# Optimization experiments

Hardware: AMD Instinct MI355X
Metric: run time of the kernel (lower is better)

## Reference

```python
import jax, jax.numpy as jnp
import numpy as np

N_NODES = 100000
N_EDGES = 1600000

def _graph_conv(x, src, dst, W_rel, b_rel, W_root):
    # sum-aggregate source features at destination nodes (PyG GraphConv, aggr='add')
    agg = jax.ops.segment_sum(x[src], dst, num_segments=N_NODES)  # [N, Fin]
    return agg @ W_rel.T + b_rel + x @ W_root.T  # [N, Fout]

def setup_inputs() -> dict:
    key = jax.random.key(0)
    ks = jax.random.split(key, 10)
    x = jax.random.normal(ks[0], (N_NODES, 4), dtype=jnp.float32)
    edge_index = jax.random.randint(ks[1], (2, N_EDGES), 0, N_NODES, dtype=jnp.int32)
    def lin(k, fo, fi):
        return jax.random.normal(k, (fo, fi), dtype=jnp.float32) / np.sqrt(fi)
    return {
        "x": x,
        "edge_index": edge_index,
        "W1_rel": lin(ks[2], 128, 4),
        "b1": jax.random.normal(ks[3], (128,), dtype=jnp.float32) * 0.01,
        "W1_root": lin(ks[4], 128, 4),
        "W2_rel": lin(ks[5], 128, 128),
        "b2": jax.random.normal(ks[6], (128,), dtype=jnp.float32) * 0.01,
        "W2_root": lin(ks[7], 128, 128),
        "Wlin": lin(ks[8], 2, 128),
        "blin": jax.random.normal(ks[9], (2,), dtype=jnp.float32) * 0.01,
    }

def reference(x, edge_index, W1_rel, b1, W1_root, W2_rel, b2, W2_root, Wlin, blin):
    src, dst = edge_index[0], edge_index[1]
    h = jax.nn.relu(_graph_conv(x, src, dst, W1_rel, b1, W1_root))   # [N,128]
    h = jax.nn.relu(_graph_conv(h, src, dst, W2_rel, b2, W2_root))   # [N,128]
    # global_mean_pool with batch = zeros -> mean over all nodes, single graph
    g = jnp.mean(h, axis=0, keepdims=True)                           # [1,128]
    return g @ Wlin.T + blin                                         # [1,2]
```

## Files before the change

### kernel.cpp

```cpp
#include <hip/hip_runtime.h>
#include <cstddef>

#define N_NODES 100000
#define N_EDGES 1600000
#define NCHUNK32 3125
#define BUCK_SHIFT 6
#define BUCK_NODES 64
#define NBUCK 1563
#define EB_CAP 1536
#define BF_EDGES 8192
#define BF_BLOCKS ((N_EDGES + BF_EDGES - 1) / BF_EDGES)

typedef __attribute__((ext_vector_type(8))) short short8;
typedef __attribute__((ext_vector_type(4))) float f32x4;
typedef __attribute__((ext_vector_type(2))) float f32x2;

__device__ __forceinline__ unsigned pack_bf16x2(float a, float b) {
  unsigned ua = __float_as_uint(a); ua += 0x7FFFu + ((ua >> 16) & 1u);
  unsigned ub = __float_as_uint(b); ub += 0x7FFFu + ((ub >> 16) & 1u);
  return (ua >> 16) | (ub & 0xFFFF0000u);
}

__global__ __launch_bounds__(512) void k_init(int* __restrict__ bucket_cursor,
                                              float* __restrict__ gsum,
                                              const float* __restrict__ W2_rel,
                                              const float* __restrict__ W2_root,
                                              unsigned* __restrict__ wbuf) {
  int t = threadIdx.x;
  for (int b = t; b < NBUCK; b += 512) bucket_cursor[b] = b * EB_CAP;
  if (t < 128) gsum[t] = 0.0f;
#pragma unroll
  for (int i = 0; i < 8; ++i) {
    int e = t + i * 512;
    int L = e & 63, T = (e >> 6) & 7, K0 = e >> 9;
    int f = T * 16 + (L & 15);
    int k0 = K0 * 32 + ((L >> 4) << 3);
    const float* wsrc = (k0 < 128) ? (W2_rel + f * 128 + k0)
                                   : (W2_root + f * 128 + (k0 - 128));
    float4 w0 = *(const float4*)(wsrc);
    float4 w1 = *(const float4*)(wsrc + 4);
    unsigned* d = wbuf + e * 4;
    d[0] = pack_bf16x2(w0.x, w0.y);
    d[1] = pack_bf16x2(w0.z, w0.w);
    d[2] = pack_bf16x2(w1.x, w1.y);
    d[3] = pack_bf16x2(w1.z, w1.w);
  }
}

__global__ __launch_bounds__(512) void k_bfill(const int* __restrict__ src,
                                               const int* __restrict__ dst,
                                               int* __restrict__ bucket_cursor,
                                               unsigned* __restrict__ ebuf) {
  __shared__ int lh[NBUCK];
  __shared__ int sub_base[NBUCK];
  __shared__ int cur[NBUCK];
  int t = threadIdx.x;
  for (int b = t; b < NBUCK; b += 512) { lh[b] = 0; cur[b] = 0; }
  __syncthreads();
  int e0 = blockIdx.x * BF_EDGES;
  unsigned pk[16];
  int bk[16];
#pragma unroll
  for (int i = 0; i < 16; ++i) {
    int e = e0 + i * 512 + t;
    bk[i] = -1;
    if (e < N_EDGES) {
      int d = dst[e];
      int b = d >> BUCK_SHIFT;
      bk[i] = b;
      pk[i] = ((unsigned)(d & (BUCK_NODES - 1)) << 17) | (unsigned)src[e];
      atomicAdd(&lh[b], 1);
    }
  }
  __syncthreads();
  for (int b = t; b < NBUCK; b += 512)
    sub_base[b] = (lh[b] > 0) ? atomicAdd(&bucket_cursor[b], lh[b]) : 0;
  __syncthreads();
#pragma unroll
  for (int i = 0; i < 16; ++i) {
    if (bk[i] >= 0) {
      int pos = sub_base[bk[i]] + atomicAdd(&cur[bk[i]], 1);
      if (pos < (bk[i] + 1) * EB_CAP) ebuf[pos] = pk[i];
    }
  }
}

__global__ __launch_bounds__(256) void k_fill2(
    const unsigned* __restrict__ ebuf, const int* __restrict__ bucket_cursor,
    const float* __restrict__ x, const float* __restrict__ W1_rel,
    const float* __restrict__ b1, const float* __restrict__ W1_root,
    int* __restrict__ row_start, int* __restrict__ row_end,
    int* __restrict__ csr_src, unsigned short* __restrict__ h1f8) {
  __shared__ int cnt[BUCK_NODES];
  __shared__ int start[BUCK_NODES];
  __shared__ float sagg[BUCK_NODES * 4];
  __shared__ float sx[BUCK_NODES * 4];
  __shared__ float sWa[8 * 128];
  __shared__ float sb1[128];
  int t = threadIdx.x;
  int b = blockIdx.x;
  int base = b * EB_CAP;
  int nb = bucket_cursor[b] - base;
  if (nb > EB_CAP) nb = EB_CAP;
  int n0 = b << BUCK_SHIFT;

  if (t < 128) {
    float4 wr = *(const float4*)(W1_rel + t * 4);
    float4 wo = *(const float4*)(W1_root + t * 4);
    sWa[0 * 128 + t] = wr.x; sWa[1 * 128 + t] = wr.y;
    sWa[2 * 128 + t] = wr.z; sWa[3 * 128 + t] = wr.w;
    sWa[4 * 128 + t] = wo.x; sWa[5 * 128 + t] = wo.y;
    sWa[6 * 128 + t] = wo.z; sWa[7 * 128 + t] = wo.w;
    sb1[t] = b1[t];
  }
  if (t < BUCK_NODES) {
    cnt[t] = 0;
    float4 xv = make_float4(0.f, 0.f, 0.f, 0.f);
    if (n0 + t < N_NODES) xv = *(const float4*)(x + (size_t)(n0 + t) * 4);
    *(float4*)&sx[t * 4] = xv;
  }
  __syncthreads();

  for (int i = t; i < nb; i += 256) atomicAdd(&cnt[ebuf[base + i] >> 17], 1);
  __syncthreads();
  if (t < 64) {
    int v = cnt[t];
    int incl = v;
#pragma unroll
    for (int off = 1; off < 64; off <<= 1) {
      int nvv = __shfl_up(incl, off);
      if (t >= off) incl += nvv;
    }
    int excl = incl - v;
    start[t] = excl;
    cnt[t] = excl;
    if (n0 + t < N_NODES) row_start[n0 + t] = base + excl;
  }
  __syncthreads();
  for (int i = t; i < nb; i += 256) {
    unsigned e = ebuf[base + i];
    int p = atomicAdd(&cnt[e >> 17], 1);
    csr_src[base + p] = (int)(e & 0x1FFFFu);
  }
  __syncthreads();
  {
    int nd = t >> 2, sub = t & 3;
    int rs = base + start[nd];
    int re = base + cnt[nd];
    float4 acc = make_float4(0.f, 0.f, 0.f, 0.f);
    for (int i = rs + sub; i < re; i += 4) {
      int s = csr_src[i];
      float4 v = *(const float4*)(x + (size_t)s * 4);
      acc.x += v.x; acc.y += v.y; acc.z += v.z; acc.w += v.w;
    }
#pragma unroll
    for (int off = 1; off < 4; off <<= 1) {
      acc.x += __shfl_xor(acc.x, off);
      acc.y += __shfl_xor(acc.y, off);
      acc.z += __shfl_xor(acc.z, off);
      acc.w += __shfl_xor(acc.w, off);
    }
    if (sub == 0) *(float4*)&sagg[nd * 4] = acc;
    if (t < 64 && n0 + t < N_NODES) row_end[n0 + t] = base + cnt[t];
  }
  __syncthreads();

  for (int it = t; it < BUCK_NODES * 64; it += 256) {
    int nd = it >> 6;
    if (n0 + nd >= N_NODES) break;
    int fp = it & 63;
    int f = fp * 2;
    float4 a  = *(float4*)&sagg[nd * 4];
    float4 xv = *(float4*)&sx[nd * 4];
    float v0 = sb1[f]
        + a.x  * sWa[0 * 128 + f] + a.y  * sWa[1 * 128 + f]
        + a.z  * sWa[2 * 128 + f] + a.w  * sWa[3 * 128 + f]
        + xv.x * sWa[4 * 128 + f] + xv.y * sWa[5 * 128 + f]
        + xv.z * sWa[6 * 128 + f] + xv.w * sWa[7 * 128 + f];
    int f1 = f + 1;
    float v1 = sb1[f1]
        + a.x  * sWa[0 * 128 + f1] + a.y  * sWa[1 * 128 + f1]
        + a.z  * sWa[2 * 128 + f1] + a.w  * sWa[3 * 128 + f1]
        + xv.x * sWa[4 * 128 + f1] + xv.y * sWa[5 * 128 + f1]
        + xv.z * sWa[6 * 128 + f1] + xv.w * sWa[7 * 128 + f1];
    float r0 = fmaxf(v0, 0.f), r1 = fmaxf(v1, 0.f);
    h1f8[(size_t)(n0 + nd) * 64 + fp] =
        (unsigned short)__builtin_amdgcn_cvt_pk_fp8_f32(r0, r1, 0, false);
  }
}

__global__ __launch_bounds__(256) void k_pull128(
    const unsigned short* __restrict__ h1f8, const int* __restrict__ row_start,
    const int* __restrict__ row_end, const int* __restrict__ csr_src,
    unsigned* __restrict__ agg2b) {
  int w = (blockIdx.x * 256 + threadIdx.x) >> 6;
  if (w >= N_NODES) return;
  int lane = threadIdx.x & 63;
  int rs = row_start[w], re = row_end[w];
  float ax = 0.f, ay = 0.f;
  for (int chunk = rs; chunk < re; chunk += 64) {
    int nv = min(64, re - chunk);
    int sv = (chunk + lane < re) ? csr_src[chunk + lane] : 0;
    int j = 0;
    for (; j + 4 <= nv; j += 4) {
      int s0 = __shfl(sv, j);
      int s1 = __shfl(sv, j + 1);
      int s2 = __shfl(sv, j + 2);
      int s3 = __shfl(sv, j + 3);
      int u0 = h1f8[(size_t)s0 * 64 + lane];
      int u1 = h1f8[(size_t)s1 * 64 + lane];
      int u2 = h1f8[(size_t)s2 * 64 + lane];
      int u3 = h1f8[(size_t)s3 * 64 + lane];
      f32x2 d0 = __builtin_amdgcn_cvt_pk_f32_fp8(u0, false);
      f32x2 d1 = __builtin_amdgcn_cvt_pk_f32_fp8(u1, false);
      f32x2 d2 = __builtin_amdgcn_cvt_pk_f32_fp8(u2, false);
      f32x2 d3 = __builtin_amdgcn_cvt_pk_f32_fp8(u3, false);
      ax += d0.x + d1.x + d2.x + d3.x;
      ay += d0.y + d1.y + d2.y + d3.y;
    }
    for (; j < nv; ++j) {
      int s0 = __shfl(sv, j);
      int u0 = h1f8[(size_t)s0 * 64 + lane];
      f32x2 d0 = __builtin_amdgcn_cvt_pk_f32_fp8(u0, false);
      ax += d0.x; ay += d0.y;
    }
  }
  agg2b[(size_t)w * 64 + lane] = pack_bf16x2(ax, ay);
}

__global__ __launch_bounds__(256) void k_gemm_pool(
    const unsigned* __restrict__ agg2b_u, const unsigned short* __restrict__ h1f8,
    const unsigned* __restrict__ wbuf_u, const float* __restrict__ b2,
    float* __restrict__ gsum) {
  __shared__ float lgs[128];
  int t = threadIdx.x;
  if (t < 128) lgs[t] = 0.0f;
  __syncthreads();

  int lane = t & 63;
  int gw = blockIdx.x * 4 + (t >> 6);
  int lrow = lane & 15;
  int quad = lane >> 4;
  const unsigned short* agg2b = (const unsigned short*)agg2b_u;
  const unsigned char* h8 = (const unsigned char*)h1f8;
  const short8* wb = (const short8*)wbuf_u;

  float bias[8];
#pragma unroll
  for (int tt = 0; tt < 8; ++tt) bias[tt] = b2[tt * 16 + lrow];
  float csum[8] = {0.f, 0.f, 0.f, 0.f, 0.f, 0.f, 0.f, 0.f};

  if (gw < NCHUNK32) {
    int mbase = gw * 32;

    f32x4 acc[2][8];
#pragma unroll
    for (int mt = 0; mt < 2; ++mt)
#pragma unroll
      for (int tt = 0; tt < 8; ++tt) acc[mt][tt] = (f32x4){0.f, 0.f, 0.f, 0.f};

#pragma unroll
    for (int ks = 0; ks < 4; ++ks) {
      const unsigned short* abase = agg2b + ks * 32 + quad * 8;
      short8 afr[2];
#pragma unroll
      for (int mt = 0; mt < 2; ++mt)
        afr[mt] = *(const short8*)(abase + (size_t)(mbase + mt * 16 + lrow) * 128);
      short8 bfr[8];
#pragma unroll
      for (int tt = 0; tt < 8; ++tt) bfr[tt] = wb[(ks * 8 + tt) * 64 + lane];
#pragma unroll
      for (int mt = 0; mt < 2; ++mt)
#pragma unroll
        for (int tt = 0; tt < 8; ++tt)
          acc[mt][tt] = __builtin_amdgcn_mfma_f32_16x16x32_bf16(
              afr[mt], bfr[tt], acc[mt][tt], 0, 0, 0);
    }
#pragma unroll
    for (int ks = 4; ks < 8; ++ks) {
      short8 afr[2];
#pragma unroll
      for (int mt = 0; mt < 2; ++mt) {
        const uint2* ap = (const uint2*)(h8 + (size_t)(mbase + mt * 16 + lrow) * 128
                                         + (ks - 4) * 32 + quad * 8);
        uint2 u = *ap;
        f32x2 a0 = __builtin_amdgcn_cvt_pk_f32_fp8((int)u.x, false);
        f32x2 a1 = __builtin_amdgcn_cvt_pk_f32_fp8((int)u.x, true);
        f32x2 a2 = __builtin_amdgcn_cvt_pk_f32_fp8((int)u.y, false);
        f32x2 a3 = __builtin_amdgcn_cvt_pk_f32_fp8((int)u.y, true);
        unsigned q0 = pack_bf16x2(a0.x, a0.y);
        unsigned q1 = pack_bf16x2(a1.x, a1.y);
        unsigned q2 = pack_bf16x2(a2.x, a2.y);
        unsigned q3 = pack_bf16x2(a3.x, a3.y);
        unsigned q[4] = {q0, q1, q2, q3};
        afr[mt] = *(short8*)q;
      }
      short8 bfr[8];
#pragma unroll
      for (int tt = 0; tt < 8; ++tt) bfr[tt] = wb[(ks * 8 + tt) * 64 + lane];
#pragma unroll
      for (int mt = 0; mt < 2; ++mt)
#pragma unroll
        for (int tt = 0; tt < 8; ++tt)
          acc[mt][tt] = __builtin_amdgcn_mfma_f32_16x16x32_bf16(
              afr[mt], bfr[tt], acc[mt][tt], 0, 0, 0);
    }

#pragma unroll
    for (int mt = 0; mt < 2; ++mt) {
#pragma unroll
      for (int tt = 0; tt < 8; ++tt) {
        f32x4 v = acc[mt][tt];
        float s = fmaxf(v.x + bias[tt], 0.f) + fmaxf(v.y + bias[tt], 0.f)
                + fmaxf(v.z + bias[tt], 0.f) + fmaxf(v.w + bias[tt], 0.f);
        s += __shfl_xor(s, 16);
        s += __shfl_xor(s, 32);
        csum[tt] += s;
      }
    }
  }
  if (lane < 16) {
#pragma unroll
    for (int tt = 0; tt < 8; ++tt) atomicAdd(&lgs[tt * 16 + lane], csum[tt]);
  }
  __syncthreads();
  if (t < 128) atomicAdd(&gsum[t], lgs[t]);
}

__global__ void k_final(const float* __restrict__ gsum, const float* __restrict__ Wlin,
                        const float* __restrict__ blin, float* __restrict__ out) {
  int lane = threadIdx.x;
  float g0 = gsum[lane];
  float g1 = gsum[lane + 64];
  float s0 = g0 * Wlin[lane]       + g1 * Wlin[lane + 64];
  float s1 = g0 * Wlin[128 + lane] + g1 * Wlin[192 + lane];
#pragma unroll
  for (int off = 32; off > 0; off >>= 1) {
    s0 += __shfl_down(s0, off);
    s1 += __shfl_down(s1, off);
  }
  if (lane == 0) {
    const float inv = 1.0f / (float)N_NODES;
    out[0] = s0 * inv + blin[0];
    out[1] = s1 * inv + blin[1];
  }
}

extern "C" void kernel_launch(void* const* d_in, const int* in_sizes, int n_in,
                              void* d_out, int out_size, void* d_ws, size_t ws_size,
                              hipStream_t stream) {
  const float* x       = (const float*)d_in[0];
  const int*   ei      = (const int*)d_in[1];
  const float* W1_rel  = (const float*)d_in[2];
  const float* b1      = (const float*)d_in[3];
  const float* W1_root = (const float*)d_in[4];
  const float* W2_rel  = (const float*)d_in[5];
  const float* b2      = (const float*)d_in[6];
  const float* W2_root = (const float*)d_in[7];
  const float* Wlin    = (const float*)d_in[8];
  const float* blin    = (const float*)d_in[9];
  const int* src = ei;
  const int* dst = ei + N_EDGES;
  float* out = (float*)d_out;

  char* ws = (char*)d_ws;
  int*            row_start     = (int*)(ws);
  int*            row_end       = (int*)(ws + 400000);
  int*            bucket_cursor = (int*)(ws + 800000);
  float*          gsum          = (float*)(ws + 808192);
  unsigned*       wbuf          = (unsigned*)(ws + 808704);
  int*            csr_src       = (int*)(ws + 874240);
  unsigned*       ebuf          = (unsigned*)(ws + 10477312);
  unsigned short* h1f8          = (unsigned short*)(ws + 20080384);
  unsigned*       agg2b         = (unsigned*)(ws + 32880384);

  k_init <<<1, 512, 0, stream>>>(bucket_cursor, gsum, W2_rel, W2_root, wbuf);
  k_bfill<<<BF_BLOCKS, 512, 0, stream>>>(src, dst, bucket_cursor, ebuf);
  k_fill2<<<NBUCK, 256, 0, stream>>>(ebuf, bucket_cursor, x, W1_rel, b1, W1_root,
                                     row_start, row_end, csr_src, h1f8);
  k_pull128<<<(N_NODES * 64 + 255) / 256, 256, 0, stream>>>(h1f8, row_start, row_end,
                                                            csr_src, agg2b);
  k_gemm_pool<<<(NCHUNK32 + 3) / 4, 256, 0, stream>>>(agg2b, h1f8, wbuf, b2, gsum);
  k_final<<<1, 64, 0, stream>>>(gsum, Wlin, blin, out);
}
```

Baseline: 212.6 us.

## Split pull wave into half-waves with 4-byte gathers; fuse final reduction into GEMM

The neighbor-aggregation kernel now has each half-wave handle a different source edge, with every lane loading 4 fp8 features (uint) instead of 2. The two halves are combined with a cross-half shuffle at the end. This halves the gather instructions per edge and doubles the bytes per load. Separately, the final linear layer moves into the GEMM/pool kernel through a last-block-done atomic counter, which removes one kernel launch at the cost of a threadfence and an atomic per block.

```diff
diff --git a/kernel.cpp b/kernel.cpp
--- a/kernel.cpp
+++ b/kernel.cpp
@@ -4,6 +4,7 @@
 #define N_NODES 100000
 #define N_EDGES 1600000
 #define NCHUNK32 3125
+#define GEMM_BLOCKS ((NCHUNK32 + 3) / 4)
 #define BUCK_SHIFT 6
 #define BUCK_NODES 64
 #define NBUCK 1563
@@ -23,12 +24,14 @@
 
 __global__ __launch_bounds__(512) void k_init(int* __restrict__ bucket_cursor,
                                               float* __restrict__ gsum,
+                                              int* __restrict__ done,
                                               const float* __restrict__ W2_rel,
                                               const float* __restrict__ W2_root,
                                               unsigned* __restrict__ wbuf) {
   int t = threadIdx.x;
   for (int b = t; b < NBUCK; b += 512) bucket_cursor[b] = b * EB_CAP;
   if (t < 128) gsum[t] = 0.0f;
+  if (t == 0) *done = 0;
 #pragma unroll
   for (int i = 0; i < 8; ++i) {
     int e = t + i * 512;
@@ -190,49 +193,79 @@
 }
 
 __global__ __launch_bounds__(256) void k_pull128(
-    const unsigned short* __restrict__ h1f8, const int* __restrict__ row_start,
+    const unsigned* __restrict__ h1f8_u, const int* __restrict__ row_start,
     const int* __restrict__ row_end, const int* __restrict__ csr_src,
-    unsigned* __restrict__ agg2b) {
+    uint2* __restrict__ agg2b) {
   int w = (blockIdx.x * 256 + threadIdx.x) >> 6;
   if (w >= N_NODES) return;
   int lane = threadIdx.x & 63;
+  int half = lane >> 5;
+  int hl = lane & 31;
   int rs = row_start[w], re = row_end[w];
-  float ax = 0.f, ay = 0.f;
+  float a0 = 0.f, a1 = 0.f, a2 = 0.f, a3 = 0.f;
   for (int chunk = rs; chunk < re; chunk += 64) {
     int nv = min(64, re - chunk);
     int sv = (chunk + lane < re) ? csr_src[chunk + lane] : 0;
     int j = 0;
-    for (; j + 4 <= nv; j += 4) {
+    for (; j + 8 <= nv; j += 8) {
+      int s0 = __shfl(sv, j + 0 + half);
+      int s1 = __shfl(sv, j + 2 + half);
+      int s2 = __shfl(sv, j + 4 + half);
+      int s3 = __shfl(sv, j + 6 + half);
+      unsigned u0 = h1f8_u[(size_t)s0 * 32 + hl];
+      unsigned u1 = h1f8_u[(size_t)s1 * 32 + hl];
+      unsigned u2 = h1f8_u[(size_t)s2 * 32 + hl];
+      unsigned u3 = h1f8_u[(size_t)s3 * 32 + hl];
+      f32x2 l0 = __builtin_amdgcn_cvt_pk_f32_fp8((int)u0, false);
+      f32x2 h0 = __builtin_amdgcn_cvt_pk_f32_fp8((int)u0, true);
+      f32x2 l1 = __builtin_amdgcn_cvt_pk_f32_fp8((int)u1, false);
+      f32x2 h1 = __builtin_amdgcn_cvt_pk_f32_fp8((int)u1, true);
+      f32x2 l2 = __builtin_amdgcn_cvt_pk_f32_fp8((int)u2, false);
+      f32x2 h2 = __builtin_amdgcn_cvt_pk_f32_fp8((int)u2, true);
+      f32x2 l3 = __builtin_amdgcn_cvt_pk_f32_fp8((int)u3, false);
+      f32x2 h3 = __builtin_amdgcn_cvt_pk_f32_fp8((int)u3, true);
+      a0 += l0.x + l1.x + l2.x + l3.x;
+      a1 += l0.y + l1.y + l2.y + l3.y;
+      a2 += h0.x + h1.x + h2.x + h3.x;
+      a3 += h0.y + h1.y + h2.y + h3.y;
+    }
+    for (; j + 2 <= nv; j += 2) {
+      int s0 = __shfl(sv, j + half);
+      unsigned u0 = h1f8_u[(size_t)s0 * 32 + hl];
+      f32x2 l0 = __builtin_amdgcn_cvt_pk_f32_fp8((int)u0, false);
+      f32x2 h0 = __builtin_amdgcn_cvt_pk_f32_fp8((int)u0, true);
+      a0 += l0.x; a1 += l0.y; a2 += h0.x; a3 += h0.y;
+    }
+    if (j < nv) {
       int s0 = __shfl(sv, j);
-      int s1 = __shfl(sv, j + 1);
-      int s2 = __shfl(sv, j + 2);
-      int s3 = __shfl(sv, j + 3);
-      int u0 = h1f8[(size_t)s0 * 64 + lane];
-      int u1 = h1f8[(size_t)s1 * 64 + lane];
-      int u2 = h1f8[(size_t)s2 * 64 + lane];
-      int u3 = h1f8[(size_t)s3 * 64 + lane];
-      f32x2 d0 = __builtin_amdgcn_cvt_pk_f32_fp8(u0, false);
-      f32x2 d1 = __builtin_amdgcn_cvt_pk_f32_fp8(u1, false);
-      f32x2 d2 = __builtin_amdgcn_cvt_pk_f32_fp8(u2, false);
-      f32x2 d3 = __builtin_amdgcn_cvt_pk_f32_fp8(u3, false);
-      ax += d0.x + d1.x + d2.x + d3.x;
-      ay += d0.y + d1.y + d2.y + d3.y;
-    }
-    for (; j < nv; ++j) {
-      int s0 = __shfl(sv, j);
-      int u0 = h1f8[(size_t)s0 * 64 + lane];
-      f32x2 d0 = __builtin_amdgcn_cvt_pk_f32_fp8(u0, false);
-      ax += d0.x; ay += d0.y;
-    }
-  }
-  agg2b[(size_t)w * 64 + lane] = pack_bf16x2(ax, ay);
+      unsigned u0 = h1f8_u[(size_t)s0 * 32 + hl];
+      if (half == 0) {
+        f32x2 l0 = __builtin_amdgcn_cvt_pk_f32_fp8((int)u0, false);
+        f32x2 h0 = __builtin_amdgcn_cvt_pk_f32_fp8((int)u0, true);
+        a0 += l0.x; a1 += l0.y; a2 += h0.x; a3 += h0.y;
+      }
+    }
+  }
+  a0 += __shfl_xor(a0, 32);
+  a1 += __shfl_xor(a1, 32);
+  a2 += __shfl_xor(a2, 32);
+  a3 += __shfl_xor(a3, 32);
+  if (half == 0) {
+    uint2 o;
+    o.x = pack_bf16x2(a0, a1);
+    o.y = pack_bf16x2(a2, a3);
+    agg2b[(size_t)w * 32 + hl] = o;
+  }
 }
 
 __global__ __launch_bounds__(256) void k_gemm_pool(
     const unsigned* __restrict__ agg2b_u, const unsigned short* __restrict__ h1f8,
     const unsigned* __restrict__ wbuf_u, const float* __restrict__ b2,
-    float* __restrict__ gsum) {
+    float* __restrict__ gsum, int* __restrict__ done,
+    const float* __restrict__ Wlin, const float* __restrict__ blin,
+    float* __restrict__ out) {
   __shared__ float lgs[128];
+  __shared__ int amlast;
   int t = threadIdx.x;
   if (t < 128) lgs[t] = 0.0f;
   __syncthreads();
@@ -288,11 +321,8 @@
         f32x2 a1 = __builtin_amdgcn_cvt_pk_f32_fp8((int)u.x, true);
         f32x2 a2 = __builtin_amdgcn_cvt_pk_f32_fp8((int)u.y, false);
         f32x2 a3 = __builtin_amdgcn_cvt_pk_f32_fp8((int)u.y, true);
-        unsigned q0 = pack_bf16x2(a0.x, a0.y);
-        unsigned q1 = pack_bf16x2(a1.x, a1.y);
-        unsigned q2 = pack_bf16x2(a2.x, a2.y);
-        unsigned q3 = pack_bf16x2(a3.x, a3.y);
-        unsigned q[4] = {q0, q1, q2, q3};
+        unsigned q[4] = {pack_bf16x2(a0.x, a0.y), pack_bf16x2(a1.x, a1.y),
+                         pack_bf16x2(a2.x, a2.y), pack_bf16x2(a3.x, a3.y)};
         afr[mt] = *(short8*)q;
       }
       short8 bfr[8];
@@ -325,24 +355,25 @@
   }
   __syncthreads();
   if (t < 128) atomicAdd(&gsum[t], lgs[t]);
-}
-
-__global__ void k_final(const float* __restrict__ gsum, const float* __restrict__ Wlin,
-                        const float* __restrict__ blin, float* __restrict__ out) {
-  int lane = threadIdx.x;
-  float g0 = gsum[lane];
-  float g1 = gsum[lane + 64];
-  float s0 = g0 * Wlin[lane]       + g1 * Wlin[lane + 64];
-  float s1 = g0 * Wlin[128 + lane] + g1 * Wlin[192 + lane];
-#pragma unroll
-  for (int off = 32; off > 0; off >>= 1) {
-    s0 += __shfl_down(s0, off);
-    s1 += __shfl_down(s1, off);
-  }
-  if (lane == 0) {
-    const float inv = 1.0f / (float)N_NODES;
-    out[0] = s0 * inv + blin[0];
-    out[1] = s1 * inv + blin[1];
+
+  __threadfence();
+  if (t == 0) amlast = (atomicAdd(done, 1) == (int)gridDim.x - 1);
+  __syncthreads();
+  if (amlast && t < 64) {
+    float g0 = atomicAdd(&gsum[t], 0.0f);
+    float g1 = atomicAdd(&gsum[t + 64], 0.0f);
+    float s0 = g0 * Wlin[t]       + g1 * Wlin[t + 64];
+    float s1 = g0 * Wlin[128 + t] + g1 * Wlin[192 + t];
+#pragma unroll
+    for (int off = 32; off > 0; off >>= 1) {
+      s0 += __shfl_down(s0, off);
+      s1 += __shfl_down(s1, off);
+    }
+    if (t == 0) {
+      const float inv = 1.0f / (float)N_NODES;
+      out[0] = s0 * inv + blin[0];
+      out[1] = s1 * inv + blin[1];
+    }
   }
 }
 
@@ -368,18 +399,19 @@
   int*            row_end       = (int*)(ws + 400000);
   int*            bucket_cursor = (int*)(ws + 800000);
   float*          gsum          = (float*)(ws + 808192);
-  unsigned*       wbuf          = (unsigned*)(ws + 808704);
-  int*            csr_src       = (int*)(ws + 874240);
-  unsigned*       ebuf          = (unsigned*)(ws + 10477312);
-  unsigned short* h1f8          = (unsigned short*)(ws + 20080384);
-  unsigned*       agg2b         = (unsigned*)(ws + 32880384);
-
-  k_init <<<1, 512, 0, stream>>>(bucket_cursor, gsum, W2_rel, W2_root, wbuf);
+  int*            done          = (int*)(ws + 808704);
+  unsigned*       wbuf          = (unsigned*)(ws + 808832);
+  int*            csr_src       = (int*)(ws + 874368);
+  unsigned*       ebuf          = (unsigned*)(ws + 10477440);
+  unsigned short* h1f8          = (unsigned short*)(ws + 20080512);
+  uint2*          agg2b         = (uint2*)(ws + 32880512);
+
+  k_init <<<1, 512, 0, stream>>>(bucket_cursor, gsum, done, W2_rel, W2_root, wbuf);
   k_bfill<<<BF_BLOCKS, 512, 0, stream>>>(src, dst, bucket_cursor, ebuf);
   k_fill2<<<NBUCK, 256, 0, stream>>>(ebuf, bucket_cursor, x, W1_rel, b1, W1_root,
                                      row_start, row_end, csr_src, h1f8);
-  k_pull128<<<(N_NODES * 64 + 255) / 256, 256, 0, stream>>>(h1f8, row_start, row_end,
-                                                            csr_src, agg2b);
-  k_gemm_pool<<<(NCHUNK32 + 3) / 4, 256, 0, stream>>>(agg2b, h1f8, wbuf, b2, gsum);
-  k_final<<<1, 64, 0, stream>>>(gsum, Wlin, blin, out);
-}
+  k_pull128<<<(N_NODES * 64 + 255) / 256, 256, 0, stream>>>(
+      (const unsigned*)h1f8, row_start, row_end, csr_src, agg2b);
+  k_gemm_pool<<<GEMM_BLOCKS, 256, 0, stream>>>(
+      (const unsigned*)agg2b, h1f8, wbuf, b2, gsum, done, Wlin, blin, out);
+}
```

Measured after the change: 232.9 us. 1.1x slower.

## Widen gather loads, store aggregated features as fp8, pack row bounds

Applied to the files above, without the earlier changes.

The pull kernel now has each lane load 8 fp8 features (uint2) while four edges are processed per wave at once, then reduces across quarter-waves. The aggregated layer-2 input is stored as fp8 instead of bf16, which halves its write and read traffic in the GEMM, and the GEMM loop is unified over both fp8 operands. Row start/end are packed into an int2, and the edge bucketing kernel reads src/dst with int4 vector loads. The cost is extra precision loss from quantising sums of up to ~16+ fp8 values back to fp8, plus cross-lane shuffles.

```diff
diff --git a/kernel.cpp b/kernel.cpp
--- a/kernel.cpp
+++ b/kernel.cpp
@@ -4,6 +4,7 @@
 #define N_NODES 100000
 #define N_EDGES 1600000
 #define NCHUNK32 3125
+#define GEMM_BLOCKS ((NCHUNK32 + 3) / 4)
 #define BUCK_SHIFT 6
 #define BUCK_NODES 64
 #define NBUCK 1563
@@ -61,15 +62,32 @@
   unsigned pk[16];
   int bk[16];
 #pragma unroll
-  for (int i = 0; i < 16; ++i) {
-    int e = e0 + i * 512 + t;
-    bk[i] = -1;
-    if (e < N_EDGES) {
-      int d = dst[e];
-      int b = d >> BUCK_SHIFT;
-      bk[i] = b;
-      pk[i] = ((unsigned)(d & (BUCK_NODES - 1)) << 17) | (unsigned)src[e];
-      atomicAdd(&lh[b], 1);
+  for (int i = 0; i < 4; ++i) {
+    int e = e0 + (i * 512 + t) * 4;
+    if (e + 4 <= N_EDGES) {
+      int4 s4 = *(const int4*)(src + e);
+      int4 d4 = *(const int4*)(dst + e);
+      int dd[4] = {d4.x, d4.y, d4.z, d4.w};
+      int ss[4] = {s4.x, s4.y, s4.z, s4.w};
+#pragma unroll
+      for (int j = 0; j < 4; ++j) {
+        int b = dd[j] >> BUCK_SHIFT;
+        bk[i * 4 + j] = b;
+        pk[i * 4 + j] = ((unsigned)(dd[j] & (BUCK_NODES - 1)) << 17) | (unsigned)ss[j];
+        atomicAdd(&lh[b], 1);
+      }
+    } else {
+#pragma unroll
+      for (int j = 0; j < 4; ++j) {
+        bk[i * 4 + j] = -1;
+        if (e + j < N_EDGES) {
+          int d = dst[e + j];
+          int b = d >> BUCK_SHIFT;
+          bk[i * 4 + j] = b;
+          pk[i * 4 + j] = ((unsigned)(d & (BUCK_NODES - 1)) << 17) | (unsigned)src[e + j];
+          atomicAdd(&lh[b], 1);
+        }
+      }
     }
   }
   __syncthreads();
@@ -89,8 +107,8 @@
     const unsigned* __restrict__ ebuf, const int* __restrict__ bucket_cursor,
     const float* __restrict__ x, const float* __restrict__ W1_rel,
     const float* __restrict__ b1, const float* __restrict__ W1_root,
-    int* __restrict__ row_start, int* __restrict__ row_end,
-    int* __restrict__ csr_src, unsigned short* __restrict__ h1f8) {
+    int2* __restrict__ row_se, int* __restrict__ csr_src,
+    unsigned short* __restrict__ h1f8) {
   __shared__ int cnt[BUCK_NODES];
   __shared__ int start[BUCK_NODES];
   __shared__ float sagg[BUCK_NODES * 4];
@@ -134,7 +152,6 @@
     int excl = incl - v;
     start[t] = excl;
     cnt[t] = excl;
-    if (n0 + t < N_NODES) row_start[n0 + t] = base + excl;
   }
   __syncthreads();
   for (int i = t; i < nb; i += 256) {
@@ -161,7 +178,8 @@
       acc.w += __shfl_xor(acc.w, off);
     }
     if (sub == 0) *(float4*)&sagg[nd * 4] = acc;
-    if (t < 64 && n0 + t < N_NODES) row_end[n0 + t] = base + cnt[t];
+    if (t < 64 && n0 + t < N_NODES)
+      row_se[n0 + t] = make_int2(base + start[t], base + cnt[t]);
   }
   __syncthreads();
 
@@ -190,46 +208,71 @@
 }
 
 __global__ __launch_bounds__(256) void k_pull128(
-    const unsigned short* __restrict__ h1f8, const int* __restrict__ row_start,
-    const int* __restrict__ row_end, const int* __restrict__ csr_src,
-    unsigned* __restrict__ agg2b) {
+    const unsigned* __restrict__ h1f8_u, const int2* __restrict__ row_se,
+    const int* __restrict__ csr_src, uint2* __restrict__ aggf8) {
   int w = (blockIdx.x * 256 + threadIdx.x) >> 6;
   if (w >= N_NODES) return;
   int lane = threadIdx.x & 63;
-  int rs = row_start[w], re = row_end[w];
-  float ax = 0.f, ay = 0.f;
+  int q = lane >> 4;
+  int ql = lane & 15;
+  int2 se = row_se[w];
+  int rs = se.x, re = se.y;
+  const uint2* hrow = (const uint2*)h1f8_u;
+  float a0=0.f,a1=0.f,a2=0.f,a3=0.f,a4=0.f,a5=0.f,a6=0.f,a7=0.f;
   for (int chunk = rs; chunk < re; chunk += 64) {
     int nv = min(64, re - chunk);
     int sv = (chunk + lane < re) ? csr_src[chunk + lane] : 0;
     int j = 0;
-    for (; j + 4 <= nv; j += 4) {
-      int s0 = __shfl(sv, j);
-      int s1 = __shfl(sv, j + 1);
-      int s2 = __shfl(sv, j + 2);
-      int s3 = __shfl(sv, j + 3);
-      int u0 = h1f8[(size_t)s0 * 64 + lane];
-      int u1 = h1f8[(size_t)s1 * 64 + lane];
-      int u2 = h1f8[(size_t)s2 * 64 + lane];
-      int u3 = h1f8[(size_t)s3 * 64 + lane];
-      f32x2 d0 = __builtin_amdgcn_cvt_pk_f32_fp8(u0, false);
-      f32x2 d1 = __builtin_amdgcn_cvt_pk_f32_fp8(u1, false);
-      f32x2 d2 = __builtin_amdgcn_cvt_pk_f32_fp8(u2, false);
-      f32x2 d3 = __builtin_amdgcn_cvt_pk_f32_fp8(u3, false);
-      ax += d0.x + d1.x + d2.x + d3.x;
-      ay += d0.y + d1.y + d2.y + d3.y;
-    }
-    for (; j < nv; ++j) {
-      int s0 = __shfl(sv, j);
-      int u0 = h1f8[(size_t)s0 * 64 + lane];
-      f32x2 d0 = __builtin_amdgcn_cvt_pk_f32_fp8(u0, false);
-      ax += d0.x; ay += d0.y;
-    }
-  }
-  agg2b[(size_t)w * 64 + lane] = pack_bf16x2(ax, ay);
+    for (; j + 8 <= nv; j += 8) {
+      int sA = __shfl(sv, j + q);
+      int sB = __shfl(sv, j + 4 + q);
+      uint2 uA = hrow[(size_t)sA * 16 + ql];
+      uint2 uB = hrow[(size_t)sB * 16 + ql];
+      f32x2 pA0 = __builtin_amdgcn_cvt_pk_f32_fp8((int)uA.x, false);
+      f32x2 pA1 = __builtin_amdgcn_cvt_pk_f32_fp8((int)uA.x, true);
+      f32x2 pA2 = __builtin_amdgcn_cvt_pk_f32_fp8((int)uA.y, false);
+      f32x2 pA3 = __builtin_amdgcn_cvt_pk_f32_fp8((int)uA.y, true);
+      f32x2 pB0 = __builtin_amdgcn_cvt_pk_f32_fp8((int)uB.x, false);
+      f32x2 pB1 = __builtin_amdgcn_cvt_pk_f32_fp8((int)uB.x, true);
+      f32x2 pB2 = __builtin_amdgcn_cvt_pk_f32_fp8((int)uB.y, false);
+      f32x2 pB3 = __builtin_amdgcn_cvt_pk_f32_fp8((int)uB.y, true);
+      a0 += pA0.x + pB0.x;  a1 += pA0.y + pB0.y;
+      a2 += pA1.x + pB1.x;  a3 += pA1.y + pB1.y;
+      a4 += pA2.x + pB2.x;  a5 += pA2.y + pB2.y;
+      a6 += pA3.x + pB3.x;  a7 += pA3.y + pB3.y;
+    }
+    for (; j < nv; j += 4) {
+      int idx = j + q;
+      int s = __shfl(sv, (idx < nv) ? idx : 0);
+      uint2 u = hrow[(size_t)s * 16 + ql];
+      if (idx >= nv) { u.x = 0u; u.y = 0u; }
+      f32x2 p0 = __builtin_amdgcn_cvt_pk_f32_fp8((int)u.x, false);
+      f32x2 p1 = __builtin_amdgcn_cvt_pk_f32_fp8((int)u.x, true);
+      f32x2 p2 = __builtin_amdgcn_cvt_pk_f32_fp8((int)u.y, false);
+      f32x2 p3 = __builtin_amdgcn_cvt_pk_f32_fp8((int)u.y, true);
+      a0 += p0.x; a1 += p0.y; a2 += p1.x; a3 += p1.y;
+      a4 += p2.x; a5 += p2.y; a6 += p3.x; a7 += p3.y;
+    }
+  }
+  a0 += __shfl_xor(a0, 16); a1 += __shfl_xor(a1, 16);
+  a2 += __shfl_xor(a2, 16); a3 += __shfl_xor(a3, 16);
+  a4 += __shfl_xor(a4, 16); a5 += __shfl_xor(a5, 16);
+  a6 += __shfl_xor(a6, 16); a7 += __shfl_xor(a7, 16);
+  a0 += __shfl_xor(a0, 32); a1 += __shfl_xor(a1, 32);
+  a2 += __shfl_xor(a2, 32); a3 += __shfl_xor(a3, 32);
+  a4 += __shfl_xor(a4, 32); a5 += __shfl_xor(a5, 32);
+  a6 += __shfl_xor(a6, 32); a7 += __shfl_xor(a7, 32);
+  if (lane < 16) {
+    unsigned lo = __builtin_amdgcn_cvt_pk_fp8_f32(a0, a1, 0, false);
+    lo = __builtin_amdgcn_cvt_pk_fp8_f32(a2, a3, lo, true);
+    unsigned hi = __builtin_amdgcn_cvt_pk_fp8_f32(a4, a5, 0, false);
+    hi = __builtin_amdgcn_cvt_pk_fp8_f32(a6, a7, hi, true);
+    aggf8[(size_t)w * 16 + ql] = make_uint2(lo, hi);
+  }
 }
 
 __global__ __launch_bounds__(256) void k_gemm_pool(
-    const unsigned* __restrict__ agg2b_u, const unsigned short* __restrict__ h1f8,
+    const unsigned* __restrict__ aggf8_u, const unsigned short* __restrict__ h1f8,
     const unsigned* __restrict__ wbuf_u, const float* __restrict__ b2,
     float* __restrict__ gsum) {
   __shared__ float lgs[128];
@@ -241,7 +284,7 @@
   int gw = blockIdx.x * 4 + (t >> 6);
   int lrow = lane & 15;
   int quad = lane >> 4;
-  const unsigned short* agg2b = (const unsigned short*)agg2b_u;
+  const unsigned char* g8 = (const unsigned char*)aggf8_u;
   const unsigned char* h8 = (const unsigned char*)h1f8;
   const short8* wb = (const short8*)wbuf_u;
 
@@ -260,40 +303,21 @@
       for (int tt = 0; tt < 8; ++tt) acc[mt][tt] = (f32x4){0.f, 0.f, 0.f, 0.f};
 
 #pragma unroll
-    for (int ks = 0; ks < 4; ++ks) {
-      const unsigned short* abase = agg2b + ks * 32 + quad * 8;
+    for (int ks = 0; ks < 8; ++ks) {
+      const unsigned char* ab = (ks < 4) ? g8 : h8;
+      int koff = (ks & 3) * 32 + quad * 8;
       short8 afr[2];
 #pragma unroll
-      for (int mt = 0; mt < 2; ++mt)
-        afr[mt] = *(const short8*)(abase + (size_t)(mbase + mt * 16 + lrow) * 128);
-      short8 bfr[8];
-#pragma unroll
-      for (int tt = 0; tt < 8; ++tt) bfr[tt] = wb[(ks * 8 + tt) * 64 + lane];
-#pragma unroll
-      for (int mt = 0; mt < 2; ++mt)
-#pragma unroll
-        for (int tt = 0; tt < 8; ++tt)
-          acc[mt][tt] = __builtin_amdgcn_mfma_f32_16x16x32_bf16(
-              afr[mt], bfr[tt], acc[mt][tt], 0, 0, 0);
-    }
-#pragma unroll
-    for (int ks = 4; ks < 8; ++ks) {
-      short8 afr[2];
-#pragma unroll
       for (int mt = 0; mt < 2; ++mt) {
-        const uint2* ap = (const uint2*)(h8 + (size_t)(mbase + mt * 16 + lrow) * 128
-                                         + (ks - 4) * 32 + quad * 8);
+        const uint2* ap = (const uint2*)(ab + (size_t)(mbase + mt * 16 + lrow) * 128 + koff);
         uint2 u = *ap;
         f32x2 a0 = __builtin_amdgcn_cvt_pk_f32_fp8((int)u.x, false);
         f32x2 a1 = __builtin_amdgcn_cvt_pk_f32_fp8((int)u.x, true);
         f32x2 a2 = __builtin_amdgcn_cvt_pk_f32_fp8((int)u.y, false);
         f32x2 a3 = __builtin_amdgcn_cvt_pk_f32_fp8((int)u.y, true);
-        unsigned q0 = pack_bf16x2(a0.x, a0.y);
-        unsigned q1 = pack_bf16x2(a1.x, a1.y);
-        unsigned q2 = pack_bf16x2(a2.x, a2.y);
-        unsigned q3 = pack_bf16x2(a3.x, a3.y);
-        unsigned q[4] = {q0, q1, q2, q3};
-        afr[mt] = *(short8*)q;
+        unsigned qq[4] = {pack_bf16x2(a0.x, a0.y), pack_bf16x2(a1.x, a1.y),
+                          pack_bf16x2(a2.x, a2.y), pack_bf16x2(a3.x, a3.y)};
+        afr[mt] = *(short8*)qq;
       }
       short8 bfr[8];
 #pragma unroll
@@ -364,22 +388,22 @@
   float* out = (float*)d_out;
 
   char* ws = (char*)d_ws;
-  int*            row_start     = (int*)(ws);
-  int*            row_end       = (int*)(ws + 400000);
+  int2*           row_se        = (int2*)(ws);
   int*            bucket_cursor = (int*)(ws + 800000);
   float*          gsum          = (float*)(ws + 808192);
-  unsigned*       wbuf          = (unsigned*)(ws + 808704);
-  int*            csr_src       = (int*)(ws + 874240);
-  unsigned*       ebuf          = (unsigned*)(ws + 10477312);
-  unsigned short* h1f8          = (unsigned short*)(ws + 20080384);
-  unsigned*       agg2b         = (unsigned*)(ws + 32880384);
+  unsigned*       wbuf          = (unsigned*)(ws + 808832);
+  int*            csr_src       = (int*)(ws + 874368);
+  unsigned*       ebuf          = (unsigned*)(ws + 10477440);
+  unsigned short* h1f8          = (unsigned short*)(ws + 20080512);
+  uint2*          aggf8         = (uint2*)(ws + 32880512);
 
   k_init <<<1, 512, 0, stream>>>(bucket_cursor, gsum, W2_rel, W2_root, wbuf);
   k_bfill<<<BF_BLOCKS, 512, 0, stream>>>(src, dst, bucket_cursor, ebuf);
   k_fill2<<<NBUCK, 256, 0, stream>>>(ebuf, bucket_cursor, x, W1_rel, b1, W1_root,
-                                     row_start, row_end, csr_src, h1f8);
-  k_pull128<<<(N_NODES * 64 + 255) / 256, 256, 0, stream>>>(h1f8, row_start, row_end,
-                                                            csr_src, agg2b);
-  k_gemm_pool<<<(NCHUNK32 + 3) / 4, 256, 0, stream>>>(agg2b, h1f8, wbuf, b2, gsum);
+                                     row_se, csr_src, h1f8);
+  k_pull128<<<(N_NODES * 64 + 255) / 256, 256, 0, stream>>>(
+      (const unsigned*)h1f8, row_se, csr_src, aggf8);
+  k_gemm_pool<<<GEMM_BLOCKS, 256, 0, stream>>>(
+      (const unsigned*)aggf8, h1f8, wbuf, b2, gsum);
   k_final<<<1, 64, 0, stream>>>(gsum, Wlin, blin, out);
 }
```

New measurement: 207.0 us. -2.6%, faster.
